# Optimization experiments

Measured on AMD Instinct MI355X. Metric: run time of the kernel, lower is better.

## Reference

```python
import jax, jax.numpy as jnp
import numpy as np

B, S, D, H = 2, 2048, 1024, 16
HD = D // H  # head dim = 64


def setup_inputs() -> dict:
    key = jax.random.key(0)
    k1, k2, k3, k4 = jax.random.split(key, 4)
    x = jax.random.normal(k1, (B, S, D), dtype=jnp.float32)
    context = jax.random.normal(k2, (B, S, D), dtype=jnp.float32)
    Wq = jax.random.normal(k3, (D, D), dtype=jnp.float32) * 0.02   # to_query weight [out,in]
    Wkv = jax.random.normal(k4, (2 * D, D), dtype=jnp.float32) * 0.02  # to_key_value weight [out,in]
    return {"x": x, "context": context, "Wq": Wq, "Wkv": Wkv}


def reference(x, context, Wq, Wkv):
    b, i, _ = x.shape
    j = context.shape[1]
    # projections (torch Linear: y = x @ W.T)
    q = x @ Wq.T                      # [b, i, D]
    kv = context @ Wkv.T              # [b, j, 2D]
    k, v = kv[..., :D], kv[..., D:]
    # split heads: (h c) ordering -> reshape last dim to [H, HD]
    q = q.reshape(b, i, H, HD).transpose(0, 2, 1, 3)  # [b,h,i,c]
    k = k.reshape(b, j, H, HD).transpose(0, 2, 1, 3)  # [b,h,j,c]
    v = v.reshape(b, j, H, HD).transpose(0, 2, 1, 3)  # [b,h,j,c]
    q = q * (HD ** -0.5)
    scores = jnp.einsum('bhic,bhjc->bhij', q, k)      # [b,h,i,j]
    scores = scores - jax.lax.stop_gradient(scores.max(axis=-1, keepdims=True))
    attn = jax.nn.softmax(scores, axis=-1)
    out = jnp.einsum('bhij,bhjc->bhic', attn, v)      # [b,h,i,c]
    out = out.transpose(0, 2, 1, 3).reshape(b, i, H * HD)  # 'b h n d -> b n (h d)'
    return out
```

## Files before the change

### kernel.cpp

```cpp
#include <hip/hip_runtime.h>
#include <hip/hip_bf16.h>
#include <stdint.h>

typedef unsigned short u16;
typedef __attribute__((ext_vector_type(8))) __bf16 bf16x8;
typedef __attribute__((ext_vector_type(4))) float f32x4;
typedef __attribute__((ext_vector_type(16))) float f32x16;

#define AS1(p) ((const __attribute__((address_space(1))) void*)(p))
#define AS3(p) ((__attribute__((address_space(3))) void*)(p))

__device__ __forceinline__ u16 f2bf(float f) {
  union { float f; uint32_t u; } c; c.f = f;
  uint32_t u = c.u;
  u += 0x7fffu + ((u >> 16) & 1u);
  return (u16)(u >> 16);
}

__device__ __forceinline__ float exp2_fast(float x) {
  float r; asm("v_exp_f32 %0, %1" : "=v"(r) : "v"(x)); return r;
}

__global__ __launch_bounds__(256) void cast4_f32_bf16(
    const float4* __restrict__ s0, ushort4* __restrict__ d0, int n0,
    const float4* __restrict__ s1, ushort4* __restrict__ d1, int n1,
    const float4* __restrict__ s2, ushort4* __restrict__ d2, int n2,
    const float4* __restrict__ s3, ushort4* __restrict__ d3, int n3) {
  int bid = blockIdx.x;
  const float4* src; ushort4* dst; int n4, b0, nb;
  if (bid < 512)       { src = s0; dst = d0; n4 = n0; b0 = 0;    nb = 512; }
  else if (bid < 1024) { src = s1; dst = d1; n4 = n1; b0 = 512;  nb = 512; }
  else if (bid < 1152) { src = s2; dst = d2; n4 = n2; b0 = 1024; nb = 128; }
  else                 { src = s3; dst = d3; n4 = n3; b0 = 1152; nb = 256; }
  int stride = nb * 256;
  for (int i = (bid - b0) * 256 + threadIdx.x; i < n4; i += stride) {
    float4 v = src[i];
    ushort4 o;
    o.x = f2bf(v.x); o.y = f2bf(v.y); o.z = f2bf(v.z); o.w = f2bf(v.w);
    dst[i] = o;
  }
}

__global__ __launch_bounds__(256) void gemm_fused(const u16* __restrict__ xb,
                                                  const u16* __restrict__ wqb,
                                                  u16* __restrict__ qo,
                                                  const u16* __restrict__ cb,
                                                  const u16* __restrict__ wkb,
                                                  u16* __restrict__ kvo,
                                                  float scale_q) {
  __shared__ u16 As[2][128 * 32];
  __shared__ u16 Bs[2][128 * 32];
  const int K = 1024;
  int bid = blockIdx.x;
  const u16 *A, *B; u16* C; int N, bm, bn; float scale;
  if (bid < 256) { A = xb; B = wqb; C = qo;  N = 1024; bm = bid >> 3; bn = bid & 7;  scale = scale_q; }
  else { int b2 = bid - 256; A = cb; B = wkb; C = kvo; N = 2048; bm = b2 >> 4; bn = b2 & 15; scale = 1.0f; }

  int tid = threadIdx.x;
  int w = tid >> 6, l = tid & 63;
  int wr = w >> 1, wc = w & 1;
  int lr = l & 15, lg = l >> 4;

  const u16* Abase = A + (size_t)(bm * 128 + (l >> 2)) * K + (l & 3) * 8;
  const u16* Bbase = B + (size_t)(bn * 128 + (l >> 2)) * K + (l & 3) * 8;

  f32x4 acc[4][4];
#pragma unroll
  for (int i = 0; i < 4; ++i)
#pragma unroll
    for (int j = 0; j < 4; ++j) acc[i][j] = (f32x4){0.f, 0.f, 0.f, 0.f};

#define STAGE(buf, k0)                                                              \
  {                                                                                 \
    _Pragma("unroll")                                                               \
    for (int t2 = 0; t2 < 2; ++t2) {                                                \
      int seg = w * 2 + t2;                                                         \
      __builtin_amdgcn_global_load_lds(AS1(Abase + (size_t)seg * 16 * K + (k0)),    \
                                       AS3(&As[buf][seg * 512]), 16, 0, 0);         \
      __builtin_amdgcn_global_load_lds(AS1(Bbase + (size_t)seg * 16 * K + (k0)),    \
                                       AS3(&Bs[buf][seg * 512]), 16, 0, 0);         \
    }                                                                               \
  }

  STAGE(0, 0);
  for (int t = 0; t < 32; ++t) {
    int cur = t & 1;
    if (t < 31) {
      STAGE(cur ^ 1, (t + 1) * 32);
      asm volatile("s_waitcnt vmcnt(4)" ::: "memory");
    } else {
      asm volatile("s_waitcnt vmcnt(0)" ::: "memory");
    }
    __builtin_amdgcn_s_barrier();
    bf16x8 af[4], bb[4];
#pragma unroll
    for (int i = 0; i < 4; ++i)
      af[i] = *(const bf16x8*)(&As[cur][(wr * 64 + i * 16 + lr) * 32 + lg * 8]);
#pragma unroll
    for (int j = 0; j < 4; ++j)
      bb[j] = *(const bf16x8*)(&Bs[cur][(wc * 64 + j * 16 + lr) * 32 + lg * 8]);
    asm volatile("s_waitcnt lgkmcnt(0)" ::: "memory");
    __builtin_amdgcn_sched_barrier(0);
#pragma unroll
    for (int i = 0; i < 4; ++i)
#pragma unroll
      for (int j = 0; j < 4; ++j)
        acc[i][j] = __builtin_amdgcn_mfma_f32_16x16x32_bf16(af[i], bb[j], acc[i][j], 0, 0, 0);
    __builtin_amdgcn_s_barrier();
  }
#undef STAGE

#pragma unroll
  for (int i = 0; i < 4; ++i)
#pragma unroll
    for (int j = 0; j < 4; ++j)
#pragma unroll
      for (int r = 0; r < 4; ++r) {
        int row = bm * 128 + wr * 64 + i * 16 + lg * 4 + r;
        int col = bn * 128 + wc * 64 + j * 16 + lr;
        C[(size_t)row * N + col] = f2bf(acc[i][j][r] * scale);
      }
}

#define SQ 2048

__global__ __launch_bounds__(256, 2) void attn_kernel(const u16* __restrict__ Q,
                                                      const u16* __restrict__ KV,
                                                      float* __restrict__ O) {
  __shared__ u16 Ks[2 * 64 * 64];
  __shared__ u16 Vt[2 * 64 * 64];

  int qt = blockIdx.x & 15;
  int bh = blockIdx.x >> 4;
  int b = bh >> 4, h = bh & 15;
  int tid = threadIdx.x;
  int w = tid >> 6, l = tid & 63;
  int li = l & 31, hi = l >> 5;
  int jr = l >> 3, bk = l & 7;

  const u16* kbase = KV + (size_t)b * SQ * 2048 + (size_t)h * 64;
  const u16* vbase = kbase + 1024;
  int i0g = qt * 128 + w * 32;
  const u16* qrow = Q + (size_t)(b * SQ + i0g + li) * 1024 + h * 64;

  bf16x8 qf0 = *(const bf16x8*)(qrow + 0  + hi * 8);
  bf16x8 qf1 = *(const bf16x8*)(qrow + 16 + hi * 8);
  bf16x8 qf2 = *(const bf16x8*)(qrow + 32 + hi * 8);
  bf16x8 qf3 = *(const bf16x8*)(qrow + 48 + hi * 8);

  {
    const u16* gk0 = kbase + (size_t)(w * 8 + jr) * 2048 + ((bk ^ jr) * 8);
    __builtin_amdgcn_global_load_lds(AS1(gk0), AS3(Ks + w * 512), 16, 0, 0);
    const u16* gk1 = kbase + (size_t)(32 + w * 8 + jr) * 2048 + ((bk ^ jr) * 8);
    __builtin_amdgcn_global_load_lds(AS1(gk1), AS3(Ks + 2048 + w * 512), 16, 0, 0);
  }
  uint4 vregA = *(const uint4*)(vbase + (size_t)(tid >> 3) * 2048 + (tid & 7) * 8);
  uint4 vregB = *(const uint4*)(vbase + (size_t)(32 + (tid >> 3)) * 2048 + (tid & 7) * 8);

  float m_run = -1e30f, l_run = 0.f;
  f32x16 acc0, acc1;
#pragma unroll
  for (int r = 0; r < 16; ++r) { acc0[r] = 0.f; acc1[r] = 0.f; }

  for (int t = 0; t < SQ / 64; ++t) {
    int cur = t & 1;
    u16* Ksc = Ks + cur * 4096;
    u16* Vtc = Vt + cur * 4096;
    __syncthreads();
    {
      int a = tid & 7, jj0 = tid >> 3;
      const u16* pa_ = (const u16*)&vregA;
#pragma unroll
      for (int e = 0; e < 8; ++e)
        *(u16*)((char*)Vtc + (a * 8 + e) * 128 + ((jj0 * 2) ^ ((e ^ a) << 4))) = pa_[e];
      const u16* pb_ = (const u16*)&vregB;
      int jj1 = 32 + jj0;
#pragma unroll
      for (int e = 0; e < 8; ++e)
        *(u16*)((char*)Vtc + (a * 8 + e) * 128 + ((jj1 * 2) ^ ((e ^ a) << 4))) = pb_[e];
    }
    __syncthreads();
    if (t + 1 < SQ / 64) {
      int nxt = cur ^ 1;
      int j0n = (t + 1) * 64;
      const u16* gk0 = kbase + (size_t)(j0n + w * 8 + jr) * 2048 + ((bk ^ jr) * 8);
      __builtin_amdgcn_global_load_lds(AS1(gk0), AS3(Ks + nxt * 4096 + w * 512), 16, 0, 0);
      const u16* gk1 = kbase + (size_t)(j0n + 32 + w * 8 + jr) * 2048 + ((bk ^ jr) * 8);
      __builtin_amdgcn_global_load_lds(AS1(gk1), AS3(Ks + nxt * 4096 + 2048 + w * 512), 16, 0, 0);
      vregA = *(const uint4*)(vbase + (size_t)(j0n + (tid >> 3)) * 2048 + (tid & 7) * 8);
      vregB = *(const uint4*)(vbase + (size_t)(j0n + 32 + (tid >> 3)) * 2048 + (tid & 7) * 8);
    }
    f32x16 s0, s1;
#pragma unroll
    for (int r = 0; r < 16; ++r) { s0[r] = 0.f; s1[r] = 0.f; }
    int swk = (li & 7) << 4;
    __builtin_amdgcn_s_setprio(1);
#pragma unroll
    for (int kb = 0; kb < 4; ++kb) {
      bf16x8 k0 = *(const bf16x8*)((const char*)Ksc + li * 128        + ((kb * 32 + hi * 16) ^ swk));
      bf16x8 k1 = *(const bf16x8*)((const char*)Ksc + (32 + li) * 128 + ((kb * 32 + hi * 16) ^ swk));
      bf16x8 qq = (kb == 0) ? qf0 : (kb == 1) ? qf1 : (kb == 2) ? qf2 : qf3;
      s0 = __builtin_amdgcn_mfma_f32_32x32x16_bf16(k0, qq, s0, 0, 0, 0);
      s1 = __builtin_amdgcn_mfma_f32_32x32x16_bf16(k1, qq, s1, 0, 0, 0);
    }
    __builtin_amdgcn_s_setprio(0);
    float pm = fmaxf(s0[0], s0[1]);
#pragma unroll
    for (int r = 2; r < 16; r += 2) pm = fmaxf(fmaxf(pm, s0[r]), s0[r + 1]);
#pragma unroll
    for (int r = 0; r < 16; r += 2) pm = fmaxf(fmaxf(pm, s1[r]), s1[r + 1]);
    pm = fmaxf(pm, __shfl_xor(pm, 32));
    if (!__all(pm <= m_run + 8.0f)) {
      float mnew = fmaxf(m_run, pm);
      float esc = exp2_fast(m_run - mnew);
      m_run = mnew;
      l_run *= esc;
#pragma unroll
      for (int r = 0; r < 16; ++r) { acc0[r] *= esc; acc1[r] *= esc; }
    }
    float p0[16], p1[16];
    float sum = 0.f;
#pragma unroll
    for (int r = 0; r < 16; ++r) { p0[r] = exp2_fast(s0[r] - m_run); sum += p0[r]; }
#pragma unroll
    for (int r = 0; r < 16; ++r) { p1[r] = exp2_fast(s1[r] - m_run); sum += p1[r]; }
    sum += __shfl_xor(sum, 32);
    l_run += sum;
    unsigned pw[16];
#pragma unroll
    for (int i2 = 0; i2 < 8; ++i2) {
      asm("v_cvt_pk_bf16_f32 %0, %1, %2" : "=v"(pw[i2])     : "v"(p0[2 * i2]), "v"(p0[2 * i2 + 1]));
      asm("v_cvt_pk_bf16_f32 %0, %1, %2" : "=v"(pw[8 + i2]) : "v"(p1[2 * i2]), "v"(p1[2 * i2 + 1]));
    }
#pragma unroll
    for (int gB = 0; gB < 2; ++gB) {
      int o = gB * 8;
      asm volatile("v_permlane32_swap_b32 %0, %1" : "+v"(pw[o + 0]), "+v"(pw[o + 2]));
      asm volatile("v_permlane32_swap_b32 %0, %1" : "+v"(pw[o + 1]), "+v"(pw[o + 3]));
      asm volatile("v_permlane32_swap_b32 %0, %1" : "+v"(pw[o + 4]), "+v"(pw[o + 6]));
      asm volatile("v_permlane32_swap_b32 %0, %1" : "+v"(pw[o + 5]), "+v"(pw[o + 7]));
    }
    __builtin_amdgcn_s_setprio(1);
#pragma unroll
    for (int kb2 = 0; kb2 < 4; ++kb2) {
      uint4 ufr;
      ufr.x = pw[kb2 * 4 + 0]; ufr.y = pw[kb2 * 4 + 1];
      ufr.z = pw[kb2 * 4 + 2]; ufr.w = pw[kb2 * 4 + 3];
      bf16x8 pa = *(bf16x8*)&ufr;
      int jbyte = kb2 * 32 + hi * 16;
      int d0_ = li, d1_ = 32 + li;
      bf16x8 v0 = *(const bf16x8*)((const char*)Vtc + d0_ * 128 + (jbyte ^ (((d0_ ^ (d0_ >> 3)) & 7) << 4)));
      bf16x8 v1 = *(const bf16x8*)((const char*)Vtc + d1_ * 128 + (jbyte ^ (((d1_ ^ (d1_ >> 3)) & 7) << 4)));
      acc0 = __builtin_amdgcn_mfma_f32_32x32x16_bf16(v0, pa, acc0, 0, 0, 0);
      acc1 = __builtin_amdgcn_mfma_f32_32x32x16_bf16(v1, pa, acc1, 0, 0, 0);
    }
    __builtin_amdgcn_s_setprio(0);
  }
  float inv = 1.f / l_run;
  float* orow = O + ((size_t)(b * SQ + i0g + li) * 1024 + h * 64);
#pragma unroll
  for (int g = 0; g < 4; ++g) {
    f32x4 o0, o1;
#pragma unroll
    for (int q_ = 0; q_ < 4; ++q_) {
      o0[q_] = acc0[g * 4 + q_] * inv;
      o1[q_] = acc1[g * 4 + q_] * inv;
    }
    *(f32x4*)(orow + 8 * g + 4 * hi) = o0;
    *(f32x4*)(orow + 32 + 8 * g + 4 * hi) = o1;
  }
}

extern "C" void kernel_launch(void* const* d_in, const int* in_sizes, int n_in,
                              void* d_out, int out_size, void* d_ws, size_t ws_size,
                              hipStream_t stream) {
  (void)in_sizes; (void)n_in; (void)out_size; (void)ws_size;
  const float* x   = (const float*)d_in[0];
  const float* ctx = (const float*)d_in[1];
  const float* Wq  = (const float*)d_in[2];
  const float* Wkv = (const float*)d_in[3];
  float* out = (float*)d_out;
  char* ws = (char*)d_ws;

  u16* xb  = (u16*)(ws);
  u16* cb  = (u16*)(ws + (8ull  << 20));
  u16* wqb = (u16*)(ws + (16ull << 20));
  u16* wkb = (u16*)(ws + (18ull << 20));
  u16* q   = (u16*)(ws + (22ull << 20));
  u16* kv  = (u16*)(ws + (30ull << 20));

  cast4_f32_bf16<<<1408, 256, 0, stream>>>(
      (const float4*)x,   (ushort4*)xb,  (4096 * 1024) / 4,
      (const float4*)ctx, (ushort4*)cb,  (4096 * 1024) / 4,
      (const float4*)Wq,  (ushort4*)wqb, (1024 * 1024) / 4,
      (const float4*)Wkv, (ushort4*)wkb, (2048 * 1024) / 4);

  gemm_fused<<<768, 256, 0, stream>>>(xb, wqb, q, cb, wkb, kv, 0.125f * 1.44269504f);

  attn_kernel<<<512, 256, 0, stream>>>(q, kv, out);
}
```

Measured before the change: 114.1 us.

## Software-pipeline attention loop: overlap next tile's QK^T with current softmax/PV

Restructures the attention KV loop so that the QK^T MFMAs for tile t+1 are issued before the softmax and PV work for tile t. It uses two ping-ponged score register sets, and the loop is unrolled by two with a prologue and an epilogue. It also merges the V-transpose store and the next-tile prefetch into one stage, cutting one __syncthreads per iteration. The aim is to hide exp and permute latency behind matrix work. The cost is 32 more live fp32 score registers per lane, which may cause spilling or lower occupancy under the two-blocks-per-CU launch bound.

```diff
diff --git a/kernel.cpp b/kernel.cpp
--- a/kernel.cpp
+++ b/kernel.cpp
@@ -123,6 +123,7 @@
 }
 
 #define SQ 2048
+#define NT 32
 
 __global__ __launch_bounds__(256, 2) void attn_kernel(const u16* __restrict__ Q,
                                                       const u16* __restrict__ KV,
@@ -162,37 +163,34 @@
 #pragma unroll
   for (int r = 0; r < 16; ++r) { acc0[r] = 0.f; acc1[r] = 0.f; }
 
-  for (int t = 0; t < SQ / 64; ++t) {
-    int cur = t & 1;
-    u16* Ksc = Ks + cur * 4096;
-    u16* Vtc = Vt + cur * 4096;
-    __syncthreads();
-    {
-      int a = tid & 7, jj0 = tid >> 3;
-      const u16* pa_ = (const u16*)&vregA;
-#pragma unroll
-      for (int e = 0; e < 8; ++e)
-        *(u16*)((char*)Vtc + (a * 8 + e) * 128 + ((jj0 * 2) ^ ((e ^ a) << 4))) = pa_[e];
-      const u16* pb_ = (const u16*)&vregB;
-      int jj1 = 32 + jj0;
-#pragma unroll
-      for (int e = 0; e < 8; ++e)
-        *(u16*)((char*)Vtc + (a * 8 + e) * 128 + ((jj1 * 2) ^ ((e ^ a) << 4))) = pb_[e];
-    }
-    __syncthreads();
-    if (t + 1 < SQ / 64) {
-      int nxt = cur ^ 1;
+  auto stage_pf = [&](int t) {
+    u16* Vtc = Vt + (t & 1) * 4096;
+    int a = tid & 7, jj0 = tid >> 3;
+    const u16* pa_ = (const u16*)&vregA;
+#pragma unroll
+    for (int e = 0; e < 8; ++e)
+      *(u16*)((char*)Vtc + (a * 8 + e) * 128 + ((jj0 * 2) ^ ((e ^ a) << 4))) = pa_[e];
+    const u16* pb_ = (const u16*)&vregB;
+    int jj1 = 32 + jj0;
+#pragma unroll
+    for (int e = 0; e < 8; ++e)
+      *(u16*)((char*)Vtc + (a * 8 + e) * 128 + ((jj1 * 2) ^ ((e ^ a) << 4))) = pb_[e];
+    if (t + 1 < NT) {
       int j0n = (t + 1) * 64;
+      u16* Ksn = Ks + ((t + 1) & 1) * 4096;
       const u16* gk0 = kbase + (size_t)(j0n + w * 8 + jr) * 2048 + ((bk ^ jr) * 8);
-      __builtin_amdgcn_global_load_lds(AS1(gk0), AS3(Ks + nxt * 4096 + w * 512), 16, 0, 0);
+      __builtin_amdgcn_global_load_lds(AS1(gk0), AS3(Ksn + w * 512), 16, 0, 0);
       const u16* gk1 = kbase + (size_t)(j0n + 32 + w * 8 + jr) * 2048 + ((bk ^ jr) * 8);
-      __builtin_amdgcn_global_load_lds(AS1(gk1), AS3(Ks + nxt * 4096 + 2048 + w * 512), 16, 0, 0);
+      __builtin_amdgcn_global_load_lds(AS1(gk1), AS3(Ksn + 2048 + w * 512), 16, 0, 0);
       vregA = *(const uint4*)(vbase + (size_t)(j0n + (tid >> 3)) * 2048 + (tid & 7) * 8);
       vregB = *(const uint4*)(vbase + (size_t)(j0n + 32 + (tid >> 3)) * 2048 + (tid & 7) * 8);
     }
-    f32x16 s0, s1;
-#pragma unroll
-    for (int r = 0; r < 16; ++r) { s0[r] = 0.f; s1[r] = 0.f; }
+  };
+
+  auto qkt = [&](int t, f32x16& n0, f32x16& n1) {
+    const u16* Ksc = Ks + (t & 1) * 4096;
+#pragma unroll
+    for (int r = 0; r < 16; ++r) { n0[r] = 0.f; n1[r] = 0.f; }
     int swk = (li & 7) << 4;
     __builtin_amdgcn_s_setprio(1);
 #pragma unroll
@@ -200,30 +198,20 @@
       bf16x8 k0 = *(const bf16x8*)((const char*)Ksc + li * 128        + ((kb * 32 + hi * 16) ^ swk));
       bf16x8 k1 = *(const bf16x8*)((const char*)Ksc + (32 + li) * 128 + ((kb * 32 + hi * 16) ^ swk));
       bf16x8 qq = (kb == 0) ? qf0 : (kb == 1) ? qf1 : (kb == 2) ? qf2 : qf3;
-      s0 = __builtin_amdgcn_mfma_f32_32x32x16_bf16(k0, qq, s0, 0, 0, 0);
-      s1 = __builtin_amdgcn_mfma_f32_32x32x16_bf16(k1, qq, s1, 0, 0, 0);
+      n0 = __builtin_amdgcn_mfma_f32_32x32x16_bf16(k0, qq, n0, 0, 0, 0);
+      n1 = __builtin_amdgcn_mfma_f32_32x32x16_bf16(k1, qq, n1, 0, 0, 0);
     }
     __builtin_amdgcn_s_setprio(0);
-    float pm = fmaxf(s0[0], s0[1]);
-#pragma unroll
-    for (int r = 2; r < 16; r += 2) pm = fmaxf(fmaxf(pm, s0[r]), s0[r + 1]);
-#pragma unroll
-    for (int r = 0; r < 16; r += 2) pm = fmaxf(fmaxf(pm, s1[r]), s1[r + 1]);
-    pm = fmaxf(pm, __shfl_xor(pm, 32));
-    if (!__all(pm <= m_run + 8.0f)) {
-      float mnew = fmaxf(m_run, pm);
-      float esc = exp2_fast(m_run - mnew);
-      m_run = mnew;
-      l_run *= esc;
-#pragma unroll
-      for (int r = 0; r < 16; ++r) { acc0[r] *= esc; acc1[r] *= esc; }
-    }
+  };
+
+  auto finish_pv = [&](int tp, const f32x16& sp0, const f32x16& sp1) {
+    const u16* Vtp = Vt + (tp & 1) * 4096;
     float p0[16], p1[16];
     float sum = 0.f;
 #pragma unroll
-    for (int r = 0; r < 16; ++r) { p0[r] = exp2_fast(s0[r] - m_run); sum += p0[r]; }
-#pragma unroll
-    for (int r = 0; r < 16; ++r) { p1[r] = exp2_fast(s1[r] - m_run); sum += p1[r]; }
+    for (int r = 0; r < 16; ++r) { p0[r] = exp2_fast(sp0[r] - m_run); sum += p0[r]; }
+#pragma unroll
+    for (int r = 0; r < 16; ++r) { p1[r] = exp2_fast(sp1[r] - m_run); sum += p1[r]; }
     sum += __shfl_xor(sum, 32);
     l_run += sum;
     unsigned pw[16];
@@ -249,13 +237,56 @@
       bf16x8 pa = *(bf16x8*)&ufr;
       int jbyte = kb2 * 32 + hi * 16;
       int d0_ = li, d1_ = 32 + li;
-      bf16x8 v0 = *(const bf16x8*)((const char*)Vtc + d0_ * 128 + (jbyte ^ (((d0_ ^ (d0_ >> 3)) & 7) << 4)));
-      bf16x8 v1 = *(const bf16x8*)((const char*)Vtc + d1_ * 128 + (jbyte ^ (((d1_ ^ (d1_ >> 3)) & 7) << 4)));
+      bf16x8 v0 = *(const bf16x8*)((const char*)Vtp + d0_ * 128 + (jbyte ^ (((d0_ ^ (d0_ >> 3)) & 7) << 4)));
+      bf16x8 v1 = *(const bf16x8*)((const char*)Vtp + d1_ * 128 + (jbyte ^ (((d1_ ^ (d1_ >> 3)) & 7) << 4)));
       acc0 = __builtin_amdgcn_mfma_f32_32x32x16_bf16(v0, pa, acc0, 0, 0, 0);
       acc1 = __builtin_amdgcn_mfma_f32_32x32x16_bf16(v1, pa, acc1, 0, 0, 0);
     }
     __builtin_amdgcn_s_setprio(0);
-  }
+  };
+
+  auto maxred = [&](const f32x16& n0, const f32x16& n1) {
+    float pm = fmaxf(n0[0], n0[1]);
+#pragma unroll
+    for (int r = 2; r < 16; r += 2) pm = fmaxf(fmaxf(pm, n0[r]), n0[r + 1]);
+#pragma unroll
+    for (int r = 0; r < 16; r += 2) pm = fmaxf(fmaxf(pm, n1[r]), n1[r + 1]);
+    pm = fmaxf(pm, __shfl_xor(pm, 32));
+    if (!__all(pm <= m_run + 8.0f)) {
+      float mnew = fmaxf(m_run, pm);
+      float esc = exp2_fast(m_run - mnew);
+      m_run = mnew;
+      l_run *= esc;
+#pragma unroll
+      for (int r = 0; r < 16; ++r) { acc0[r] *= esc; acc1[r] *= esc; }
+    }
+  };
+
+  f32x16 sa0, sa1, sb0, sb1;
+  __syncthreads();
+  stage_pf(0);
+  qkt(0, sa0, sa1);
+  maxred(sa0, sa1);
+  for (int t = 1; t < NT - 1; t += 2) {
+    __syncthreads();
+    stage_pf(t);
+    qkt(t, sb0, sb1);
+    finish_pv(t - 1, sa0, sa1);
+    maxred(sb0, sb1);
+    __syncthreads();
+    stage_pf(t + 1);
+    qkt(t + 1, sa0, sa1);
+    finish_pv(t, sb0, sb1);
+    maxred(sa0, sa1);
+  }
+  __syncthreads();
+  stage_pf(NT - 1);
+  qkt(NT - 1, sb0, sb1);
+  finish_pv(NT - 2, sa0, sa1);
+  maxred(sb0, sb1);
+  __syncthreads();
+  finish_pv(NT - 1, sb0, sb1);
+
   float inv = 1.f / l_run;
   float* orow = O + ((size_t)(b * SQ + i0g + li) * 1024 + h * 64);
 #pragma unroll
```

New measurement: 110.9 us. 2.8% less time.

## Give each attention wave 64 query rows with 2-wave blocks; remap block ids

Applied to the files above, without the earlier changes.

The attention kernel moves from 4 waves with 32 query rows each to 2 waves with 64 query rows each. Each K/V fragment read from LDS now feeds two MFMAs, which halves LDS traffic per FLOP, and each block runs two independent online-softmax states. The middle barrier after the V transpose is replaced by a waitcnt plus barrier placed after the QK MFMAs. Both the GEMM and attention block indices are remapped (XCD-style swizzle) so neighbouring tiles share L2. The cost is higher register pressure from four accumulators and four score tiles, and fewer waves per block.

```diff
diff --git a/kernel.cpp b/kernel.cpp
--- a/kernel.cpp
+++ b/kernel.cpp
@@ -19,6 +19,12 @@
 
 __device__ __forceinline__ float exp2_fast(float x) {
   float r; asm("v_exp_f32 %0, %1" : "=v"(r) : "v"(x)); return r;
+}
+
+__device__ __forceinline__ unsigned pkbf(float lo, float hi) {
+  unsigned r;
+  asm("v_cvt_pk_bf16_f32 %0, %1, %2" : "=v"(r) : "v"(lo), "v"(hi));
+  return r;
 }
 
 __global__ __launch_bounds__(256) void cast4_f32_bf16(
@@ -51,7 +57,7 @@
   __shared__ u16 As[2][128 * 32];
   __shared__ u16 Bs[2][128 * 32];
   const int K = 1024;
-  int bid = blockIdx.x;
+  int bid = (blockIdx.x & 7) * 96 + (blockIdx.x >> 3);
   const u16 *A, *B; u16* C; int N, bm, bn; float scale;
   if (bid < 256) { A = xb; B = wqb; C = qo;  N = 1024; bm = bid >> 3; bn = bid & 7;  scale = scale_q; }
   else { int b2 = bid - 256; A = cb; B = wkb; C = kvo; N = 2048; bm = b2 >> 4; bn = b2 & 15; scale = 1.0f; }
@@ -123,114 +129,79 @@
 }
 
 #define SQ 2048
-
-__global__ __launch_bounds__(256, 2) void attn_kernel(const u16* __restrict__ Q,
+#define NT 32
+
+__global__ __launch_bounds__(128, 2) void attn_kernel(const u16* __restrict__ Q,
                                                       const u16* __restrict__ KV,
                                                       float* __restrict__ O) {
   __shared__ u16 Ks[2 * 64 * 64];
   __shared__ u16 Vt[2 * 64 * 64];
 
-  int qt = blockIdx.x & 15;
-  int bh = blockIdx.x >> 4;
+  int wgid = (blockIdx.x & 7) * 64 + (blockIdx.x >> 3);
+  int qt = wgid & 15;
+  int bh = wgid >> 4;
   int b = bh >> 4, h = bh & 15;
   int tid = threadIdx.x;
   int w = tid >> 6, l = tid & 63;
   int li = l & 31, hi = l >> 5;
-  int jr = l >> 3, bk = l & 7;
+  int jr8 = l >> 3, bk = l & 7;
 
   const u16* kbase = KV + (size_t)b * SQ * 2048 + (size_t)h * 64;
   const u16* vbase = kbase + 1024;
-  int i0g = qt * 128 + w * 32;
-  const u16* qrow = Q + (size_t)(b * SQ + i0g + li) * 1024 + h * 64;
-
-  bf16x8 qf0 = *(const bf16x8*)(qrow + 0  + hi * 8);
-  bf16x8 qf1 = *(const bf16x8*)(qrow + 16 + hi * 8);
-  bf16x8 qf2 = *(const bf16x8*)(qrow + 32 + hi * 8);
-  bf16x8 qf3 = *(const bf16x8*)(qrow + 48 + hi * 8);
-
-  {
-    const u16* gk0 = kbase + (size_t)(w * 8 + jr) * 2048 + ((bk ^ jr) * 8);
-    __builtin_amdgcn_global_load_lds(AS1(gk0), AS3(Ks + w * 512), 16, 0, 0);
-    const u16* gk1 = kbase + (size_t)(32 + w * 8 + jr) * 2048 + ((bk ^ jr) * 8);
-    __builtin_amdgcn_global_load_lds(AS1(gk1), AS3(Ks + 2048 + w * 512), 16, 0, 0);
-  }
-  uint4 vregA = *(const uint4*)(vbase + (size_t)(tid >> 3) * 2048 + (tid & 7) * 8);
-  uint4 vregB = *(const uint4*)(vbase + (size_t)(32 + (tid >> 3)) * 2048 + (tid & 7) * 8);
-
-  float m_run = -1e30f, l_run = 0.f;
-  f32x16 acc0, acc1;
-#pragma unroll
-  for (int r = 0; r < 16; ++r) { acc0[r] = 0.f; acc1[r] = 0.f; }
-
-  for (int t = 0; t < SQ / 64; ++t) {
-    int cur = t & 1;
-    u16* Ksc = Ks + cur * 4096;
-    u16* Vtc = Vt + cur * 4096;
-    __syncthreads();
-    {
-      int a = tid & 7, jj0 = tid >> 3;
-      const u16* pa_ = (const u16*)&vregA;
-#pragma unroll
-      for (int e = 0; e < 8; ++e)
-        *(u16*)((char*)Vtc + (a * 8 + e) * 128 + ((jj0 * 2) ^ ((e ^ a) << 4))) = pa_[e];
-      const u16* pb_ = (const u16*)&vregB;
-      int jj1 = 32 + jj0;
-#pragma unroll
-      for (int e = 0; e < 8; ++e)
-        *(u16*)((char*)Vtc + (a * 8 + e) * 128 + ((jj1 * 2) ^ ((e ^ a) << 4))) = pb_[e];
-    }
-    __syncthreads();
-    if (t + 1 < SQ / 64) {
-      int nxt = cur ^ 1;
-      int j0n = (t + 1) * 64;
-      const u16* gk0 = kbase + (size_t)(j0n + w * 8 + jr) * 2048 + ((bk ^ jr) * 8);
-      __builtin_amdgcn_global_load_lds(AS1(gk0), AS3(Ks + nxt * 4096 + w * 512), 16, 0, 0);
-      const u16* gk1 = kbase + (size_t)(j0n + 32 + w * 8 + jr) * 2048 + ((bk ^ jr) * 8);
-      __builtin_amdgcn_global_load_lds(AS1(gk1), AS3(Ks + nxt * 4096 + 2048 + w * 512), 16, 0, 0);
-      vregA = *(const uint4*)(vbase + (size_t)(j0n + (tid >> 3)) * 2048 + (tid & 7) * 8);
-      vregB = *(const uint4*)(vbase + (size_t)(j0n + 32 + (tid >> 3)) * 2048 + (tid & 7) * 8);
-    }
-    f32x16 s0, s1;
-#pragma unroll
-    for (int r = 0; r < 16; ++r) { s0[r] = 0.f; s1[r] = 0.f; }
-    int swk = (li & 7) << 4;
-    __builtin_amdgcn_s_setprio(1);
-#pragma unroll
-    for (int kb = 0; kb < 4; ++kb) {
-      bf16x8 k0 = *(const bf16x8*)((const char*)Ksc + li * 128        + ((kb * 32 + hi * 16) ^ swk));
-      bf16x8 k1 = *(const bf16x8*)((const char*)Ksc + (32 + li) * 128 + ((kb * 32 + hi * 16) ^ swk));
-      bf16x8 qq = (kb == 0) ? qf0 : (kb == 1) ? qf1 : (kb == 2) ? qf2 : qf3;
-      s0 = __builtin_amdgcn_mfma_f32_32x32x16_bf16(k0, qq, s0, 0, 0, 0);
-      s1 = __builtin_amdgcn_mfma_f32_32x32x16_bf16(k1, qq, s1, 0, 0, 0);
-    }
-    __builtin_amdgcn_s_setprio(0);
-    float pm = fmaxf(s0[0], s0[1]);
-#pragma unroll
-    for (int r = 2; r < 16; r += 2) pm = fmaxf(fmaxf(pm, s0[r]), s0[r + 1]);
-#pragma unroll
-    for (int r = 0; r < 16; r += 2) pm = fmaxf(fmaxf(pm, s1[r]), s1[r + 1]);
+  int i0w = qt * 128 + w * 64;
+  const u16* qrow0 = Q + (size_t)(b * SQ + i0w + li) * 1024 + h * 64;
+  const u16* qrow1 = qrow0 + (size_t)32 * 1024;
+
+  bf16x8 qA0 = *(const bf16x8*)(qrow0 + 0  + hi * 8);
+  bf16x8 qA1 = *(const bf16x8*)(qrow0 + 16 + hi * 8);
+  bf16x8 qA2 = *(const bf16x8*)(qrow0 + 32 + hi * 8);
+  bf16x8 qA3 = *(const bf16x8*)(qrow0 + 48 + hi * 8);
+  bf16x8 qB0 = *(const bf16x8*)(qrow1 + 0  + hi * 8);
+  bf16x8 qB1 = *(const bf16x8*)(qrow1 + 16 + hi * 8);
+  bf16x8 qB2 = *(const bf16x8*)(qrow1 + 32 + hi * 8);
+  bf16x8 qB3 = *(const bf16x8*)(qrow1 + 48 + hi * 8);
+
+#pragma unroll
+  for (int c = 0; c < 4; ++c) {
+    const u16* gk = kbase + (size_t)(w * 32 + c * 8 + jr8) * 2048 + ((bk ^ jr8) * 8);
+    __builtin_amdgcn_global_load_lds(AS1(gk), AS3(Ks + w * 2048 + c * 512), 16, 0, 0);
+  }
+  uint4 vr0 = *(const uint4*)(vbase + (size_t)(0  + (tid >> 3)) * 2048 + (tid & 7) * 8);
+  uint4 vr1 = *(const uint4*)(vbase + (size_t)(16 + (tid >> 3)) * 2048 + (tid & 7) * 8);
+  uint4 vr2 = *(const uint4*)(vbase + (size_t)(32 + (tid >> 3)) * 2048 + (tid & 7) * 8);
+  uint4 vr3 = *(const uint4*)(vbase + (size_t)(48 + (tid >> 3)) * 2048 + (tid & 7) * 8);
+
+  float m0 = -1e30f, l0 = 0.f, m1 = -1e30f, l1 = 0.f;
+  f32x16 acc0, acc1, acc2, acc3;
+#pragma unroll
+  for (int r = 0; r < 16; ++r) { acc0[r] = 0.f; acc1[r] = 0.f; acc2[r] = 0.f; acc3[r] = 0.f; }
+
+  auto softmax_pack = [&](f32x16& sA, f32x16& sB, float& m, float& lsum,
+                          f32x16& aA, f32x16& aB, unsigned* pw) {
+    float pm = fmaxf(sA[0], sA[1]);
+#pragma unroll
+    for (int r = 2; r < 16; r += 2) pm = fmaxf(fmaxf(pm, sA[r]), sA[r + 1]);
+#pragma unroll
+    for (int r = 0; r < 16; r += 2) pm = fmaxf(fmaxf(pm, sB[r]), sB[r + 1]);
     pm = fmaxf(pm, __shfl_xor(pm, 32));
-    if (!__all(pm <= m_run + 8.0f)) {
-      float mnew = fmaxf(m_run, pm);
-      float esc = exp2_fast(m_run - mnew);
-      m_run = mnew;
-      l_run *= esc;
-#pragma unroll
-      for (int r = 0; r < 16; ++r) { acc0[r] *= esc; acc1[r] *= esc; }
-    }
-    float p0[16], p1[16];
+    if (!__all(pm <= m + 8.0f)) {
+      float mnew = fmaxf(m, pm);
+      float esc = exp2_fast(m - mnew);
+      m = mnew; lsum *= esc;
+#pragma unroll
+      for (int r = 0; r < 16; ++r) { aA[r] *= esc; aB[r] *= esc; }
+    }
     float sum = 0.f;
 #pragma unroll
-    for (int r = 0; r < 16; ++r) { p0[r] = exp2_fast(s0[r] - m_run); sum += p0[r]; }
-#pragma unroll
-    for (int r = 0; r < 16; ++r) { p1[r] = exp2_fast(s1[r] - m_run); sum += p1[r]; }
+    for (int r = 0; r < 16; ++r) { sA[r] = exp2_fast(sA[r] - m); sum += sA[r]; }
+#pragma unroll
+    for (int r = 0; r < 16; ++r) { sB[r] = exp2_fast(sB[r] - m); sum += sB[r]; }
     sum += __shfl_xor(sum, 32);
-    l_run += sum;
-    unsigned pw[16];
+    lsum += sum;
 #pragma unroll
     for (int i2 = 0; i2 < 8; ++i2) {
-      asm("v_cvt_pk_bf16_f32 %0, %1, %2" : "=v"(pw[i2])     : "v"(p0[2 * i2]), "v"(p0[2 * i2 + 1]));
-      asm("v_cvt_pk_bf16_f32 %0, %1, %2" : "=v"(pw[8 + i2]) : "v"(p1[2 * i2]), "v"(p1[2 * i2 + 1]));
+      pw[i2]     = pkbf(sA[2 * i2], sA[2 * i2 + 1]);
+      pw[8 + i2] = pkbf(sB[2 * i2], sB[2 * i2 + 1]);
     }
 #pragma unroll
     for (int gB = 0; gB < 2; ++gB) {
@@ -240,34 +211,98 @@
       asm volatile("v_permlane32_swap_b32 %0, %1" : "+v"(pw[o + 4]), "+v"(pw[o + 6]));
       asm volatile("v_permlane32_swap_b32 %0, %1" : "+v"(pw[o + 5]), "+v"(pw[o + 7]));
     }
+  };
+
+  for (int t = 0; t < NT; ++t) {
+    int cur = t & 1;
+    u16* Ksc = Ks + cur * 4096;
+    u16* Vtc = Vt + cur * 4096;
+    __syncthreads();
+    {
+      int a = tid & 7, jb = tid >> 3;
+      const u16* p0_ = (const u16*)&vr0;
+      const u16* p1_ = (const u16*)&vr1;
+      const u16* p2_ = (const u16*)&vr2;
+      const u16* p3_ = (const u16*)&vr3;
+#pragma unroll
+      for (int e = 0; e < 8; ++e) {
+        int dbyte = (a * 8 + e) * 128, sw = (e ^ a) << 4;
+        *(u16*)((char*)Vtc + dbyte + (((jb +  0) * 2) ^ sw)) = p0_[e];
+        *(u16*)((char*)Vtc + dbyte + (((jb + 16) * 2) ^ sw)) = p1_[e];
+        *(u16*)((char*)Vtc + dbyte + (((jb + 32) * 2) ^ sw)) = p2_[e];
+        *(u16*)((char*)Vtc + dbyte + (((jb + 48) * 2) ^ sw)) = p3_[e];
+      }
+    }
+    if (t + 1 < NT) {
+      int j0n = (t + 1) * 64;
+      u16* Ksn = Ks + (cur ^ 1) * 4096;
+#pragma unroll
+      for (int c = 0; c < 4; ++c) {
+        const u16* gk = kbase + (size_t)(j0n + w * 32 + c * 8 + jr8) * 2048 + ((bk ^ jr8) * 8);
+        __builtin_amdgcn_global_load_lds(AS1(gk), AS3(Ksn + w * 2048 + c * 512), 16, 0, 0);
+      }
+      vr0 = *(const uint4*)(vbase + (size_t)(j0n +  0 + (tid >> 3)) * 2048 + (tid & 7) * 8);
+      vr1 = *(const uint4*)(vbase + (size_t)(j0n + 16 + (tid >> 3)) * 2048 + (tid & 7) * 8);
+      vr2 = *(const uint4*)(vbase + (size_t)(j0n + 32 + (tid >> 3)) * 2048 + (tid & 7) * 8);
+      vr3 = *(const uint4*)(vbase + (size_t)(j0n + 48 + (tid >> 3)) * 2048 + (tid & 7) * 8);
+    }
+    f32x16 s0, s1, s2, s3;
+#pragma unroll
+    for (int r = 0; r < 16; ++r) { s0[r] = 0.f; s1[r] = 0.f; s2[r] = 0.f; s3[r] = 0.f; }
+    int swk = (li & 7) << 4;
     __builtin_amdgcn_s_setprio(1);
 #pragma unroll
+    for (int kb = 0; kb < 4; ++kb) {
+      bf16x8 k0 = *(const bf16x8*)((const char*)Ksc + li * 128        + ((kb * 32 + hi * 16) ^ swk));
+      bf16x8 k1 = *(const bf16x8*)((const char*)Ksc + (32 + li) * 128 + ((kb * 32 + hi * 16) ^ swk));
+      bf16x8 qa = (kb == 0) ? qA0 : (kb == 1) ? qA1 : (kb == 2) ? qA2 : qA3;
+      bf16x8 qb = (kb == 0) ? qB0 : (kb == 1) ? qB1 : (kb == 2) ? qB2 : qB3;
+      s0 = __builtin_amdgcn_mfma_f32_32x32x16_bf16(k0, qa, s0, 0, 0, 0);
+      s2 = __builtin_amdgcn_mfma_f32_32x32x16_bf16(k0, qb, s2, 0, 0, 0);
+      s1 = __builtin_amdgcn_mfma_f32_32x32x16_bf16(k1, qa, s1, 0, 0, 0);
+      s3 = __builtin_amdgcn_mfma_f32_32x32x16_bf16(k1, qb, s3, 0, 0, 0);
+    }
+    __builtin_amdgcn_s_setprio(0);
+    asm volatile("s_waitcnt lgkmcnt(0)" ::: "memory");
+    __builtin_amdgcn_s_barrier();
+    unsigned pw0[16], pw1[16];
+    softmax_pack(s0, s1, m0, l0, acc0, acc1, pw0);
+    softmax_pack(s2, s3, m1, l1, acc2, acc3, pw1);
+    __builtin_amdgcn_s_setprio(1);
+#pragma unroll
     for (int kb2 = 0; kb2 < 4; ++kb2) {
-      uint4 ufr;
-      ufr.x = pw[kb2 * 4 + 0]; ufr.y = pw[kb2 * 4 + 1];
-      ufr.z = pw[kb2 * 4 + 2]; ufr.w = pw[kb2 * 4 + 3];
-      bf16x8 pa = *(bf16x8*)&ufr;
       int jbyte = kb2 * 32 + hi * 16;
       int d0_ = li, d1_ = 32 + li;
       bf16x8 v0 = *(const bf16x8*)((const char*)Vtc + d0_ * 128 + (jbyte ^ (((d0_ ^ (d0_ >> 3)) & 7) << 4)));
       bf16x8 v1 = *(const bf16x8*)((const char*)Vtc + d1_ * 128 + (jbyte ^ (((d1_ ^ (d1_ >> 3)) & 7) << 4)));
-      acc0 = __builtin_amdgcn_mfma_f32_32x32x16_bf16(v0, pa, acc0, 0, 0, 0);
-      acc1 = __builtin_amdgcn_mfma_f32_32x32x16_bf16(v1, pa, acc1, 0, 0, 0);
+      uint4 u0; u0.x = pw0[kb2 * 4 + 0]; u0.y = pw0[kb2 * 4 + 1]; u0.z = pw0[kb2 * 4 + 2]; u0.w = pw0[kb2 * 4 + 3];
+      uint4 u1; u1.x = pw1[kb2 * 4 + 0]; u1.y = pw1[kb2 * 4 + 1]; u1.z = pw1[kb2 * 4 + 2]; u1.w = pw1[kb2 * 4 + 3];
+      bf16x8 pa0 = *(bf16x8*)&u0;
+      bf16x8 pa1 = *(bf16x8*)&u1;
+      acc0 = __builtin_amdgcn_mfma_f32_32x32x16_bf16(v0, pa0, acc0, 0, 0, 0);
+      acc2 = __builtin_amdgcn_mfma_f32_32x32x16_bf16(v0, pa1, acc2, 0, 0, 0);
+      acc1 = __builtin_amdgcn_mfma_f32_32x32x16_bf16(v1, pa0, acc1, 0, 0, 0);
+      acc3 = __builtin_amdgcn_mfma_f32_32x32x16_bf16(v1, pa1, acc3, 0, 0, 0);
     }
     __builtin_amdgcn_s_setprio(0);
   }
-  float inv = 1.f / l_run;
-  float* orow = O + ((size_t)(b * SQ + i0g + li) * 1024 + h * 64);
+  float inv0 = 1.f / l0, inv1 = 1.f / l1;
+  float* orow0 = O + ((size_t)(b * SQ + i0w + li) * 1024 + h * 64);
+  float* orow1 = orow0 + (size_t)32 * 1024;
 #pragma unroll
   for (int g = 0; g < 4; ++g) {
-    f32x4 o0, o1;
+    f32x4 oA0, oA1, oB0, oB1;
 #pragma unroll
     for (int q_ = 0; q_ < 4; ++q_) {
-      o0[q_] = acc0[g * 4 + q_] * inv;
-      o1[q_] = acc1[g * 4 + q_] * inv;
-    }
-    *(f32x4*)(orow + 8 * g + 4 * hi) = o0;
-    *(f32x4*)(orow + 32 + 8 * g + 4 * hi) = o1;
+      oA0[q_] = acc0[g * 4 + q_] * inv0;
+      oA1[q_] = acc1[g * 4 + q_] * inv0;
+      oB0[q_] = acc2[g * 4 + q_] * inv1;
+      oB1[q_] = acc3[g * 4 + q_] * inv1;
+    }
+    *(f32x4*)(orow0 + 8 * g + 4 * hi) = oA0;
+    *(f32x4*)(orow0 + 32 + 8 * g + 4 * hi) = oA1;
+    *(f32x4*)(orow1 + 8 * g + 4 * hi) = oB0;
+    *(f32x4*)(orow1 + 32 + 8 * g + 4 * hi) = oB1;
   }
 }
 
@@ -297,5 +332,5 @@
 
   gemm_fused<<<768, 256, 0, stream>>>(xb, wqb, q, cb, wkb, kv, 0.125f * 1.44269504f);
 
-  attn_kernel<<<512, 256, 0, stream>>>(q, kv, out);
-}
+  attn_kernel<<<512, 128, 0, stream>>>(q, kv, out);
+}
```

After: 138.1 us. +21.0%, slower.
